# Performance work log

Measured on AMD Instinct MI355X. Metric: run time of the kernel, lower is better.

## Reference

```python
import jax, jax.numpy as jnp
import numpy as np
from jax import lax

A = 3          # anchors per scale
C = 80         # num foreground classes (COCO)
NMS_THRESH = 0.45
NMS_TOPK = 400
POST_NMS = 100


def setup_inputs() -> dict:
    key = jax.random.key(0)
    k0, k1, k2 = jax.random.split(key, 3)
    B = 8
    ch = A * (C + 5)  # 255
    # raw head outputs (pre-decode conv activations), modest scale so exp() stays sane
    tip0 = jax.random.normal(k0, (B, ch, 19, 19), jnp.float32) * 0.5
    tip1 = jax.random.normal(k1, (B, ch, 38, 38), jnp.float32) * 0.5
    tip2 = jax.random.normal(k2, (B, ch, 76, 76), jnp.float32) * 0.5
    # standard YOLOv3 COCO anchors, deepest scale (stride 32) first
    anchors0 = jnp.array([[116., 90.], [156., 198.], [373., 326.]], jnp.float32)
    anchors1 = jnp.array([[30., 61.], [62., 45.], [59., 119.]], jnp.float32)
    anchors2 = jnp.array([[10., 13.], [16., 30.], [33., 23.]], jnp.float32)
    return dict(tip0=tip0, tip1=tip1, tip2=tip2,
                anchors0=anchors0, anchors1=anchors1, anchors2=anchors2)


def _decode(tip, anchors, stride):
    """YOLOOutputV3 inference decode. tip: (B, A*(C+5), H, W)."""
    B, _, H, W = tip.shape
    # (B, A*(C+5), H*W) -> (B, H*W, A, C+5)
    pred = tip.reshape(B, A * (C + 5), H * W).transpose(0, 2, 1).reshape(B, H * W, A, C + 5)
    gx, gy = jnp.meshgrid(jnp.arange(W), jnp.arange(H))       # each (H, W)
    offsets = jnp.stack([gx, gy], -1).reshape(1, H * W, 1, 2).astype(tip.dtype)
    centers = (jax.nn.sigmoid(pred[..., :2]) + offsets) * stride          # (B,HW,A,2)
    scales = jnp.exp(pred[..., 2:4]) * anchors.reshape(1, 1, A, 2)        # (B,HW,A,2)
    conf = jax.nn.sigmoid(pred[..., 4:5])                                 # objectness
    cls_scores = jax.nn.sigmoid(pred[..., 5:]) * conf                      # (B,HW,A,C)
    wh = scales * 0.5
    bbox = jnp.concatenate([centers - wh, centers + wh], -1)               # corner format
    return bbox.reshape(B, H * W * A, 4), cls_scores.reshape(B, H * W * A, C)


def _pairwise_iou(b):
    """b: (K,4) corner boxes -> (K,K) IoU."""
    x1, y1, x2, y2 = b[:, 0], b[:, 1], b[:, 2], b[:, 3]
    area = jnp.maximum(x2 - x1, 0.) * jnp.maximum(y2 - y1, 0.)
    iw = jnp.maximum(jnp.minimum(x2[:, None], x2[None, :]) - jnp.maximum(x1[:, None], x1[None, :]), 0.)
    ih = jnp.maximum(jnp.minimum(y2[:, None], y2[None, :]) - jnp.maximum(y1[:, None], y1[None, :]), 0.)
    inter = iw * ih
    return inter / (area[:, None] + area[None, :] - inter + 1e-12)


def _nms_single(det):
    """Class-aware greedy NMS on one image. det: (M,6) = (cid, score, x1,y1,x2,y2)."""
    K = NMS_TOPK
    _, idx = lax.top_k(det[:, 1], K)     # sort by score, keep top K
    d = det[idx]                          # (K,6), descending score
    iou = _pairwise_iou(d[:, 2:6])
    same = d[:, 0][:, None] == d[:, 0][None, :]   # only same class suppresses
    valid = d[:, 1] > 0.
    rng = jnp.arange(K)

    def body(i, keep):
        sup = (iou[i] > NMS_THRESH) & same[i] & (rng > i) & keep[i] & valid[i]
        return keep & ~sup

    keep = lax.fori_loop(0, K, body, jnp.ones((K,), bool)) & valid
    d = jnp.where(keep[:, None], d, jnp.full_like(d, -1.))
    order = jnp.argsort(-d[:, 1])         # kept (sorted) first, suppressed (-1) last
    return d[order][:POST_NMS]            # (POST_NMS, 6)


def _detect(tip0, tip1, tip2, anchors0, anchors1, anchors2):
    dets = []
    for tip, anc, stride in ((tip0, anchors0, 32), (tip1, anchors1, 16), (tip2, anchors2, 8)):
        bbox, scores = _decode(tip, anc, stride)          # (B,N,4), (B,N,C)
        B, N, _ = bbox.shape
        ids = jnp.broadcast_to(jnp.arange(C, dtype=bbox.dtype)[None, None, :, None], (B, N, C, 1))
        sc = scores[..., None]                            # (B,N,C,1)
        bx = jnp.broadcast_to(bbox[:, :, None, :], (B, N, C, 4))
        dets.append(jnp.concatenate([ids, sc, bx], -1).reshape(B, N * C, 6))
    det = jnp.concatenate(dets, 1)                        # (B, M, 6)
    return jax.vmap(_nms_single)(det)                     # (B, POST_NMS, 6)


def reference(tip0, tip1, tip2, anchors0, anchors1, anchors2):
    res = _detect(tip0, tip1, tip2, anchors0, anchors1, anchors2)
    ids = res[..., 0:1]
    scores = res[..., 1:2]
    bboxes = res[..., 2:6]
    return ids, scores, bboxes
```

## Files before the change

kernel.cpp:

```cpp
#include <hip/hip_runtime.h>
#include <stdint.h>

#define NUMA 3
#define NUMC 80
#define CAP  49152
#define KTOP 400
#define POST 100
#define EQCAP 1024
#define PFCAP 2048
#define KEY0 0x3EE66666u
#define KEYTOP 0x3F800000u
#define LBUF 1024
#define NMASK (KTOP * 7)
#define CPB 20

typedef float f32x4 __attribute__((ext_vector_type(4)));

__device__ __forceinline__ float sigmoidf_(float x) { return 1.0f / (1.0f + expf(-x)); }
__device__ __forceinline__ unsigned uminu(unsigned a, unsigned b) { return a < b ? a : b; }

__device__ __forceinline__ float thr_for(float cf) {
    if (!(cf >= 0.45f)) return 3.0e38f;
    float q = 0.449f / cf;
    float r = q / (1.0f - q);
    return logf(r) - 0.01f;
}

__global__ __launch_bounds__(256) void score_main(
        const float* __restrict__ t0, const float* __restrict__ t1,
        const float* __restrict__ t2,
        unsigned* __restrict__ ccnt, unsigned* __restrict__ ckey,
        unsigned* __restrict__ cidx)
{
    __shared__ unsigned lkey[LBUF], lidx[LBUF];
    __shared__ unsigned lcnt, lbase;
    const int tid = threadIdx.x;
    if (tid == 0) lcnt = 0;
    __syncthreads();

    const int ba = blockIdx.z;
    const int b = ba / 3, a = ba - 3 * b;
    const int c0 = blockIdx.y * CPB;
    const int cx = blockIdx.x;

    #define LEMIT(SC, IDX) do { \
        unsigned key_ = __float_as_uint(SC); \
        if (key_ >= KEY0) { \
            unsigned pos_ = atomicAdd(&lcnt, 1u); \
            if (pos_ < LBUF) { lkey[pos_] = key_; lidx[pos_] = (IDX); } \
        } \
    } while (0)

    if (cx < 2) {
        const int hw = cx * 256 + tid;
        if (hw < 361) {
            const float* base = t0 + (size_t)(b * 255 + a * 85) * 361;
            float cr = base[4 * 361 + hw];
            const float* p0 = base + (size_t)(5 + c0) * 361 + hw;
            float xv[CPB];
            #pragma unroll
            for (int u = 0; u < CPB; u++) xv[u] = p0[u * 361];
            float cf = sigmoidf_(cr);
            float xt = thr_for(cf);
            unsigned ib = (unsigned)((hw * NUMA + a) * NUMC + c0);
            #pragma unroll
            for (int u = 0; u < CPB; u++)
                if (xv[u] > xt) LEMIT(sigmoidf_(xv[u]) * cf, ib + (unsigned)u);
        }
    } else {
        const float* tip; int vHW, v, candOff;
        if (cx < 4) { tip = t1; vHW = 361;  v = (cx - 2) * 256 + tid; candOff = 86640; }
        else        { tip = t2; vHW = 1444; v = (cx - 4) * 256 + tid; candOff = 433200; }
        if (v < vHW) {
            const f32x4* bp = (const f32x4*)(tip + (size_t)(b * 255 + a * 85) * (size_t)(vHW * 4));
            f32x4 cv = bp[(size_t)4 * vHW + v];
            const f32x4* p0 = bp + (size_t)(5 + c0) * vHW + v;
            f32x4 sv[CPB];
            #pragma unroll
            for (int u = 0; u < CPB; u++) sv[u] = p0[(size_t)u * vHW];
            float cf0 = sigmoidf_(cv[0]), cf1 = sigmoidf_(cv[1]);
            float cf2 = sigmoidf_(cv[2]), cf3 = sigmoidf_(cv[3]);
            float xt0 = thr_for(cf0), xt1 = thr_for(cf1);
            float xt2 = thr_for(cf2), xt3 = thr_for(cf3);
            unsigned ib0 = (unsigned)(candOff + (v * 4 * NUMA + a) * NUMC + c0);
            #pragma unroll
            for (int u = 0; u < CPB; u++) {
                unsigned ib = ib0 + (unsigned)u;
                if (sv[u][0] > xt0) LEMIT(sigmoidf_(sv[u][0]) * cf0, ib);
                if (sv[u][1] > xt1) LEMIT(sigmoidf_(sv[u][1]) * cf1, ib + 240);
                if (sv[u][2] > xt2) LEMIT(sigmoidf_(sv[u][2]) * cf2, ib + 480);
                if (sv[u][3] > xt3) LEMIT(sigmoidf_(sv[u][3]) * cf3, ib + 720);
            }
        }
    }
    #undef LEMIT

    __syncthreads();
    if (tid == 0) {
        unsigned c = lcnt;
        if (c > LBUF) {
            atomicOr(&ccnt[b], 0x80000000u);
            lbase = 0xFFFFFFFFu;
        } else {
            lbase = atomicAdd(&ccnt[b], c);
        }
    }
    __syncthreads();
    unsigned c = uminu(lcnt, (unsigned)LBUF);
    unsigned basep = lbase;
    if (basep != 0xFFFFFFFFu) {
        for (unsigned i = tid; i < c; i += 256) {
            unsigned p = basep + i;
            if (p < CAP) {
                ckey[(size_t)b * CAP + p] = lkey[i];
                cidx[(size_t)b * CAP + p] = lidx[i];
            }
        }
    }
}

__device__ __forceinline__ void wave_select(const unsigned* h, int nbins, unsigned rank,
                                            unsigned* resv, int tid)
{
    if (tid >= 64) return;
    const int lane = tid;
    const int cs = nbins >> 6;
    unsigned v = 0;
    for (int k = 0; k < cs; k++) {
        int off = (k + lane) & (cs - 1);
        v += h[lane * cs + off];
    }
    unsigned S = v;
    #pragma unroll
    for (int o = 1; o < 64; o <<= 1) {
        unsigned t = (unsigned)__shfl_down((int)S, o);
        if (lane + o < 64) S += t;
    }
    unsigned long long bm = __ballot(S >= rank);
    if (bm == 0ull) bm = 1ull;
    int C = 63 - __builtin_clzll(bm);
    unsigned SC = (unsigned)__builtin_amdgcn_readlane((int)S, C);
    unsigned vC = (unsigned)__builtin_amdgcn_readlane((int)v, C);
    unsigned rem = rank - (SC - vC);
    unsigned w = (lane < cs) ? h[C * cs + lane] : 0u;
    unsigned T = w;
    #pragma unroll
    for (int o = 1; o < 64; o <<= 1) {
        unsigned t = (unsigned)__shfl_down((int)T, o);
        if (lane + o < 64) T += t;
    }
    unsigned long long bm2 = __ballot((T >= rem) && (lane < cs));
    if (bm2 == 0ull) bm2 = 1ull;
    int B = 63 - __builtin_clzll(bm2);
    unsigned TB = (unsigned)__builtin_amdgcn_readlane((int)T, B);
    unsigned wB = (unsigned)__builtin_amdgcn_readlane((int)w, B);
    if (lane == 0) {
        resv[0] = (unsigned)(C * cs + B);
        resv[1] = rem - (TB - wB);
    }
}

__global__ __launch_bounds__(1024) void topk_sel(
        const float* __restrict__ t0, const float* __restrict__ t1,
        const float* __restrict__ t2,
        const float* __restrict__ anc0, const float* __restrict__ anc1,
        const float* __restrict__ anc2,
        const unsigned* __restrict__ ccnt,
        unsigned* __restrict__ ckey, unsigned* __restrict__ cidx,
        float* __restrict__ dX1, float* __restrict__ dY1,
        float* __restrict__ dX2, float* __restrict__ dY2,
        float* __restrict__ dSC, unsigned* __restrict__ dCID)
{
    const int b = blockIdx.x;
    const int tid = threadIdx.x;
    const int T = 1024;

    __shared__ unsigned hist[4096];
    __shared__ unsigned resv[2];
    __shared__ unsigned selk[512], seli[512];
    __shared__ unsigned eqi[EQCAP];
    __shared__ unsigned pk[PFCAP], pi[PFCAP];
    __shared__ unsigned cnts[3];
    __shared__ unsigned fcnt;

    unsigned* ck = ckey + (size_t)b * CAP;
    unsigned* ci = cidx + (size_t)b * CAP;
    unsigned nraw = ccnt[b];
    unsigned kbase = KEY0;

    if (!(nraw >= KTOP && nraw <= CAP)) {
        const int NPOS = 3 * (361 + 1444 + 5776);
        for (int i = tid; i < 2048; i += T) hist[i] = 0;
        if (tid == 0) fcnt = 0;
        __syncthreads();
        for (int p = tid; p < NPOS; p += T) {
            const float* tip; int HW, pp;
            if (p < 1083)      { tip = t0; HW = 361;  pp = p; }
            else if (p < 5415) { tip = t1; HW = 1444; pp = p - 1083; }
            else               { tip = t2; HW = 5776; pp = p - 5415; }
            int a = pp / HW, hwl = pp - a * HW;
            const float* base = tip + (size_t)(b * 255 + a * 85) * HW;
            float cf = sigmoidf_(base[4 * HW + hwl]);
            for (int u = 0; u < NUMC; u++) {
                float sc = sigmoidf_(base[(size_t)(5 + u) * HW + hwl]) * cf;
                atomicAdd(&hist[__float_as_uint(sc) >> 19], 1u);
            }
        }
        __syncthreads();
        wave_select(hist, 2048, KTOP, resv, tid);
        __syncthreads();
        unsigned cutkey = resv[0] << 19;
        __syncthreads();
        for (int p = tid; p < NPOS; p += T) {
            const float* tip; int HW, pp, candOff;
            if (p < 1083)      { tip = t0; HW = 361;  pp = p;        candOff = 0; }
            else if (p < 5415) { tip = t1; HW = 1444; pp = p - 1083; candOff = 86640; }
            else               { tip = t2; HW = 5776; pp = p - 5415; candOff = 433200; }
            int a = pp / HW, hwl = pp - a * HW;
            const float* base = tip + (size_t)(b * 255 + a * 85) * HW;
            float cf = sigmoidf_(base[4 * HW + hwl]);
            unsigned ib0 = (unsigned)(candOff + (hwl * NUMA + a) * NUMC);
            for (int u = 0; u < NUMC; u++) {
                float sc = sigmoidf_(base[(size_t)(5 + u) * HW + hwl]) * cf;
                unsigned key = __float_as_uint(sc);
                if (key >= cutkey) {
                    unsigned pos = atomicAdd(&fcnt, 1u);
                    if (pos < CAP) { ck[pos] = key; ci[pos] = ib0 + (unsigned)u; }
                }
            }
        }
        __syncthreads();
        nraw = fcnt;
        kbase = cutkey;
    }
    unsigned n = uminu(nraw, (unsigned)CAP);

    unsigned span = (KEYTOP - kbase) + 1u;
    unsigned SH = 0;
    while ((span >> SH) > 2047u) SH++;

    for (int i = tid; i < 2048; i += T) hist[i] = 0;
    __syncthreads();
    {
        unsigned n4 = n >> 2;
        const uint4* ck4 = (const uint4*)ck;
        for (unsigned i = tid; i < n4; i += T) {
            uint4 k = ck4[i];
            atomicAdd(&hist[(k.x - kbase) >> SH], 1u);
            atomicAdd(&hist[(k.y - kbase) >> SH], 1u);
            atomicAdd(&hist[(k.z - kbase) >> SH], 1u);
            atomicAdd(&hist[(k.w - kbase) >> SH], 1u);
        }
        for (unsigned i = (n4 << 2) + tid; i < n; i += T)
            atomicAdd(&hist[(ck[i] - kbase) >> SH], 1u);
    }
    __syncthreads();
    wave_select(hist, 2048, KTOP, resv, tid);
    __syncthreads();
    unsigned Bf = resv[0];
    __syncthreads();

    if (tid == 0) { cnts[0] = 0; cnts[1] = 0; cnts[2] = 0; }
    __syncthreads();
    for (unsigned i = tid; i < n; i += T) {
        unsigned k = ck[i];
        if (((k - kbase) >> SH) >= Bf) {
            unsigned q = atomicAdd(&cnts[2], 1u);
            if (q < (unsigned)PFCAP) { pk[q] = k; pi[q] = ci[i]; }
        }
    }
    __syncthreads();
    unsigned pfCnt = cnts[2];
    bool useP = (pfCnt <= (unsigned)PFCAP);
    unsigned m = useP ? pfCnt : n;

    for (int i = tid; i < 4096; i += T) hist[i] = 0;
    __syncthreads();
    for (unsigned i = tid; i < m; i += T) {
        unsigned k = useP ? pk[i] : ck[i];
        atomicAdd(&hist[k >> 19], 1u);
    }
    __syncthreads();
    wave_select(hist, 4096, KTOP, resv, tid);
    __syncthreads();
    unsigned b1 = resv[0], r2 = resv[1];
    __syncthreads();

    for (int i = tid; i < 4096; i += T) hist[i] = 0;
    __syncthreads();
    for (unsigned i = tid; i < m; i += T) {
        unsigned k = useP ? pk[i] : ck[i];
        if ((k >> 19) == b1) atomicAdd(&hist[(k >> 7) & 0xFFFu], 1u);
    }
    __syncthreads();
    wave_select(hist, 4096, r2, resv, tid);
    __syncthreads();
    unsigned b2 = resv[0], r3 = resv[1];
    __syncthreads();

    for (int i = tid; i < 128; i += T) hist[i] = 0;
    __syncthreads();
    unsigned pref = (b1 << 12) | b2;
    for (unsigned i = tid; i < m; i += T) {
        unsigned k = useP ? pk[i] : ck[i];
        if ((k >> 7) == pref) atomicAdd(&hist[k & 127u], 1u);
    }
    __syncthreads();
    wave_select(hist, 128, r3, resv, tid);
    __syncthreads();
    unsigned b3 = resv[0], needEq = resv[1];
    unsigned K400 = (b1 << 19) | (b2 << 7) | b3;
    __syncthreads();

    for (int i = tid; i < 512; i += T) { selk[i] = 0u; seli[i] = 0xFFFFFFFFu; }
    for (int i = tid; i < EQCAP; i += T) eqi[i] = 0xFFFFFFFFu;
    __syncthreads();
    for (unsigned i = tid; i < m; i += T) {
        unsigned k = useP ? pk[i] : ck[i];
        if (k > K400) {
            unsigned idx = useP ? pi[i] : ci[i];
            unsigned p = atomicAdd(&cnts[0], 1u);
            if (p < 512u) { selk[p] = k; seli[p] = idx; }
        } else if (k == K400) {
            unsigned idx = useP ? pi[i] : ci[i];
            unsigned q = atomicAdd(&cnts[1], 1u);
            if (q < (unsigned)EQCAP) eqi[q] = idx;
        }
    }
    __syncthreads();
    unsigned selCnt = uminu(cnts[0], (unsigned)KTOP);
    unsigned eqN   = uminu(cnts[1], (unsigned)EQCAP);

    if (eqN > needEq) {
        int P2 = 1; while ((unsigned)P2 < eqN) P2 <<= 1;
        for (int k2 = 2; k2 <= P2; k2 <<= 1) {
            for (int j = k2 >> 1; j > 0; j >>= 1) {
                __syncthreads();
                for (int i = tid; i < P2; i += T) {
                    int ixj = i ^ j;
                    if (ixj > i && ixj < P2) {
                        unsigned va = eqi[i], vb = eqi[ixj];
                        bool up = ((i & k2) == 0);
                        if (up ? (va > vb) : (va < vb)) { eqi[i] = vb; eqi[ixj] = va; }
                    }
                }
            }
        }
        __syncthreads();
    }
    for (unsigned t2v = tid; t2v < needEq; t2v += T) {
        unsigned p = selCnt + t2v;
        if (p < KTOP) { selk[p] = K400; seli[p] = eqi[t2v]; }
    }
    __syncthreads();

    for (int k2 = 2; k2 <= 512; k2 <<= 1) {
        int j = k2 >> 1;
        for (; j >= 64; j >>= 1) {
            __syncthreads();
            if (tid < 512) {
                int i = tid, ixj = i ^ j;
                if (ixj > i) {
                    unsigned ka = selk[i], kb = selk[ixj], ia = seli[i], ib = seli[ixj];
                    bool before = (ka > kb) || (ka == kb && ia < ib);
                    bool up = ((i & k2) == 0);
                    if (up ? !before : before) {
                        selk[i] = kb; selk[ixj] = ka; seli[i] = ib; seli[ixj] = ia;
                    }
                }
            }
        }
        __syncthreads();
        if (tid < 512) {
            for (; j > 0; j >>= 1) {
                int i = tid, ixj = i ^ j;
                if (ixj > i) {
                    unsigned ka = selk[i], kb = selk[ixj], ia = seli[i], ib = seli[ixj];
                    bool before = (ka > kb) || (ka == kb && ia < ib);
                    bool up = ((i & k2) == 0);
                    if (up ? !before : before) {
                        selk[i] = kb; selk[ixj] = ka; seli[i] = ib; seli[ixj] = ia;
                    }
                }
            }
        }
    }
    __syncthreads();

    if (tid < KTOP) {
        unsigned idx = seli[tid];
        int o = b * KTOP + tid;
        if (idx == 0xFFFFFFFFu) {
            dX1[o] = -1.f; dY1[o] = -1.f; dX2[o] = -1.f; dY2[o] = -1.f;
            dSC[o] = __uint_as_float(selk[tid]); dCID[o] = 0u;
        } else {
            const float* tip; const float* anc; int HW, W, candOff; float strideF;
            if (idx < 86640u)       { tip = t0; anc = anc0; HW = 361;  W = 19; strideF = 32.f; candOff = 0; }
            else if (idx < 433200u) { tip = t1; anc = anc1; HW = 1444; W = 38; strideF = 16.f; candOff = 86640; }
            else                    { tip = t2; anc = anc2; HW = 5776; W = 76; strideF = 8.f;  candOff = 433200; }
            unsigned local = idx - (unsigned)candOff;
            int cls = (int)(local % NUMC);
            int nn  = (int)(local / NUMC);
            int a = nn % NUMA, hwl = nn / NUMA;
            const float* base = tip + (size_t)(b * 255 + a * 85) * HW + hwl;
            float tx = base[0];
            float ty = base[(size_t)HW];
            float tw = base[(size_t)2 * HW];
            float th = base[(size_t)3 * HW];
            float fx = (float)(hwl % W), fy = (float)(hwl / W);
            float cx = (sigmoidf_(tx) + fx) * strideF;
            float cy = (sigmoidf_(ty) + fy) * strideF;
            float hw_ = expf(tw) * anc[2 * a]     * 0.5f;
            float hh_ = expf(th) * anc[2 * a + 1] * 0.5f;
            dX1[o] = cx - hw_; dY1[o] = cy - hh_;
            dX2[o] = cx + hw_; dY2[o] = cy + hh_;
            dSC[o] = __uint_as_float(selk[tid]);
            dCID[o] = (unsigned)cls;
        }
    }
}

__global__ __launch_bounds__(256) void mask_kernel(
        const float* __restrict__ dX1, const float* __restrict__ dY1,
        const float* __restrict__ dX2, const float* __restrict__ dY2,
        const unsigned* __restrict__ dCID, unsigned long long* __restrict__ maskG)
{
    __shared__ float lx1[KTOP], ly1[KTOP], lx2[KTOP], ly2[KTOP];
    __shared__ int lcid[KTOP];
    const int b = blockIdx.y;
    const int tid = threadIdx.x;
    for (int i = tid; i < KTOP; i += 256) {
        int o = b * KTOP + i;
        lx1[i] = dX1[o]; ly1[i] = dY1[o];
        lx2[i] = dX2[o]; ly2[i] = dY2[o];
        lcid[i] = (int)dCID[o];
    }
    __syncthreads();
    int p = blockIdx.x * 256 + tid;
    if (p < NMASK) {
        int i = p / 7, w = p - i * 7;
        float x1i = lx1[i], y1i = ly1[i], x2i = lx2[i], y2i = ly2[i];
        float ai = fmaxf(x2i - x1i, 0.f) * fmaxf(y2i - y1i, 0.f);
        int cidI = lcid[i];
        unsigned long long m = 0ull;
        int j0 = w * 64;
        int rot = (9 * w) & 63;
        for (int t = 0; t < 64; t++) {
            int j = j0 + ((t + rot) & 63);
            if (j >= KTOP || j <= i) continue;
            if (lcid[j] != cidI) continue;
            float iw = fminf(x2i, lx2[j]) - fmaxf(x1i, lx1[j]);
            float ih = fminf(y2i, ly2[j]) - fmaxf(y1i, ly1[j]);
            iw = fmaxf(iw, 0.f); ih = fmaxf(ih, 0.f);
            float inter = iw * ih;
            float aj = fmaxf(lx2[j] - lx1[j], 0.f) * fmaxf(ly2[j] - ly1[j], 0.f);
            float iou = inter / (ai + aj - inter + 1e-12f);
            if (iou > 0.45f) m |= (1ull << (j - j0));
        }
        maskG[(size_t)b * NMASK + p] = m;
    }
}

__global__ __launch_bounds__(512) void greedy_kernel(
        const float* __restrict__ dX1, const float* __restrict__ dY1,
        const float* __restrict__ dX2, const float* __restrict__ dY2,
        const float* __restrict__ dSC, const unsigned* __restrict__ dCID,
        const unsigned long long* __restrict__ maskG, float* __restrict__ out)
{
    __shared__ unsigned long long maskL[NMASK];
    __shared__ unsigned long long vkeep[7];
    __shared__ float oid[POST], osc[POST], obb[POST * 4];
    const int b = blockIdx.x;
    const int tid = threadIdx.x;

    for (int i = tid; i < NMASK; i += 512) maskL[i] = maskG[(size_t)b * NMASK + i];
    if (tid < POST) { oid[tid] = -1.f; osc[tid] = -1.f; }
    if (tid < POST * 4) obb[tid] = -1.f;
    __syncthreads();

    if (tid < 64) {
        const int lane = tid;
        unsigned long long keep = 0ull;
        if (lane < 7) keep = (lane == 6) ? 0xFFFFull : ~0ull;
        unsigned long long mb[8];
        #pragma unroll
        for (int k = 0; k < 8; k++)
            mb[k] = (lane < 7) ? maskL[k * 7 + lane] : 0ull;
        for (int ib = 0; ib < KTOP; ib += 8) {
            #pragma unroll
            for (int k = 0; k < 8; k++) {
                int i = ib + k;
                unsigned long long m = mb[k];
                int nf = ib + 8 + k;
                mb[k] = (lane < 7 && nf < KTOP) ? maskL[nf * 7 + lane] : 0ull;
                int w = i >> 6;
                unsigned klo = (unsigned)__builtin_amdgcn_readlane((int)(unsigned)(keep & 0xFFFFFFFFull), w);
                unsigned khi = (unsigned)__builtin_amdgcn_readlane((int)(unsigned)(keep >> 32), w);
                unsigned long long kw = ((unsigned long long)khi << 32) | klo;
                if ((kw >> (i & 63)) & 1ull) keep &= ~m;
            }
        }
        if (lane < 7) vkeep[lane] = keep;
    }
    __syncthreads();

    if (tid < KTOP) {
        int w = tid >> 6, bp = tid & 63;
        unsigned long long kw = vkeep[w];
        if ((kw >> bp) & 1ull) {
            int r = 0;
            for (int q = 0; q < w; q++) r += __popcll(vkeep[q]);
            r += __popcll(kw & ((1ull << bp) - 1ull));
            if (r < POST) {
                int o = b * KTOP + tid;
                oid[r] = (float)(int)dCID[o];
                osc[r] = dSC[o];
                obb[r * 4 + 0] = dX1[o];
                obb[r * 4 + 1] = dY1[o];
                obb[r * 4 + 2] = dX2[o];
                obb[r * 4 + 3] = dY2[o];
            }
        }
    }
    __syncthreads();
    if (tid < POST) {
        out[b * POST + tid]       = oid[tid];
        out[800 + b * POST + tid] = osc[tid];
    }
    if (tid < POST * 4) out[1600 + b * POST * 4 + tid] = obb[tid];
}

extern "C" void kernel_launch(void* const* d_in, const int* in_sizes, int n_in,
                              void* d_out, int out_size, void* d_ws, size_t ws_size,
                              hipStream_t stream)
{
    const float* tip0 = (const float*)d_in[0];
    const float* tip1 = (const float*)d_in[1];
    const float* tip2 = (const float*)d_in[2];
    const float* anc0 = (const float*)d_in[3];
    const float* anc1 = (const float*)d_in[4];
    const float* anc2 = (const float*)d_in[5];
    float* out = (float*)d_out;

    unsigned* ccnt = (unsigned*)d_ws;
    unsigned* ckey = ccnt + 8;
    unsigned* cidx = ckey + (size_t)8 * CAP;
    float*    dX1  = (float*)(cidx + (size_t)8 * CAP);
    float*    dY1  = dX1 + 8 * KTOP;
    float*    dX2  = dY1 + 8 * KTOP;
    float*    dY2  = dX2 + 8 * KTOP;
    float*    dSC  = dY2 + 8 * KTOP;
    unsigned* dCID = (unsigned*)(dSC + 8 * KTOP);
    unsigned long long* maskG = (unsigned long long*)(dCID + 8 * KTOP);

    hipMemsetAsync(ccnt, 0, 8 * sizeof(unsigned), stream);

    dim3 g(10, 80 / CPB, 24);
    score_main<<<g, 256, 0, stream>>>(tip0, tip1, tip2, ccnt, ckey, cidx);
    topk_sel<<<8, 1024, 0, stream>>>(tip0, tip1, tip2, anc0, anc1, anc2,
                                     ccnt, ckey, cidx,
                                     dX1, dY1, dX2, dY2, dSC, dCID);
    mask_kernel<<<dim3((NMASK + 255) / 256, 8), 256, 0, stream>>>(
        dX1, dY1, dX2, dY2, dCID, maskG);
    greedy_kernel<<<8, 512, 0, stream>>>(dX1, dY1, dX2, dY2, dSC, dCID, maskG, out);
}
```

Baseline: 189.5 us.

## Build score histogram during scoring pass and replace bitonic sort with rank sort

The scoring kernel now accumulates a per-batch 2048-bin histogram of candidate keys in shared memory and merges it into global memory, so the top-k kernel can load it instead of rescanning all candidates with atomics on the common path. The bitonic sort of 512 selected keys, with its many barriers, is replaced by a rank-counting sort where each thread counts how many elements precede it and scatters directly. This adds per-block shared atomics and global histogram atomics in the scoring kernel and an O(n^2) shared-memory read loop, in exchange for fewer syncs and passes in the single-block-per-batch top-k kernel.

```diff
diff --git a/kernel.cpp b/kernel.cpp
--- a/kernel.cpp
+++ b/kernel.cpp
@@ -13,6 +13,7 @@
 #define LBUF 1024
 #define NMASK (KTOP * 7)
 #define CPB 20
+#define NBIN 2048
 
 typedef float f32x4 __attribute__((ext_vector_type(4)));
 
@@ -29,13 +30,15 @@
 __global__ __launch_bounds__(256) void score_main(
         const float* __restrict__ t0, const float* __restrict__ t1,
         const float* __restrict__ t2,
-        unsigned* __restrict__ ccnt, unsigned* __restrict__ ckey,
-        unsigned* __restrict__ cidx)
+        unsigned* __restrict__ histN, unsigned* __restrict__ ccnt,
+        unsigned* __restrict__ ckey, unsigned* __restrict__ cidx)
 {
     __shared__ unsigned lkey[LBUF], lidx[LBUF];
+    __shared__ unsigned lh[NBIN];
     __shared__ unsigned lcnt, lbase;
     const int tid = threadIdx.x;
     if (tid == 0) lcnt = 0;
+    for (int i = tid; i < NBIN; i += 256) lh[i] = 0;
     __syncthreads();
 
     const int ba = blockIdx.z;
@@ -46,6 +49,7 @@
     #define LEMIT(SC, IDX) do { \
         unsigned key_ = __float_as_uint(SC); \
         if (key_ >= KEY0) { \
+            atomicAdd(&lh[(key_ - KEY0) >> 13], 1u); \
             unsigned pos_ = atomicAdd(&lcnt, 1u); \
             if (pos_ < LBUF) { lkey[pos_] = key_; lidx[pos_] = (IDX); } \
         } \
@@ -117,6 +121,11 @@
             }
         }
     }
+    unsigned* gh = histN + b * NBIN;
+    for (int i = tid; i < NBIN; i += 256) {
+        unsigned v2 = lh[i];
+        if (v2) atomicAdd(&gh[i], v2);
+    }
 }
 
 __device__ __forceinline__ void wave_select(const unsigned* h, int nbins, unsigned rank,
@@ -165,7 +174,7 @@
         const float* __restrict__ t2,
         const float* __restrict__ anc0, const float* __restrict__ anc1,
         const float* __restrict__ anc2,
-        const unsigned* __restrict__ ccnt,
+        const unsigned* __restrict__ histN, const unsigned* __restrict__ ccnt,
         unsigned* __restrict__ ckey, unsigned* __restrict__ cidx,
         float* __restrict__ dX1, float* __restrict__ dY1,
         float* __restrict__ dX2, float* __restrict__ dY2,
@@ -178,6 +187,7 @@
     __shared__ unsigned hist[4096];
     __shared__ unsigned resv[2];
     __shared__ unsigned selk[512], seli[512];
+    __shared__ unsigned sk2[512], si2[512];
     __shared__ unsigned eqi[EQCAP];
     __shared__ unsigned pk[PFCAP], pi[PFCAP];
     __shared__ unsigned cnts[3];
@@ -187,8 +197,10 @@
     unsigned* ci = cidx + (size_t)b * CAP;
     unsigned nraw = ccnt[b];
     unsigned kbase = KEY0;
-
-    if (!(nraw >= KTOP && nraw <= CAP)) {
+    unsigned SH = 13;
+
+    bool cold = !(nraw >= KTOP && nraw <= CAP);
+    if (cold) {
         const int NPOS = 3 * (361 + 1444 + 5776);
         for (int i = tid; i < 2048; i += T) hist[i] = 0;
         if (tid == 0) fcnt = 0;
@@ -232,16 +244,15 @@
         __syncthreads();
         nraw = fcnt;
         kbase = cutkey;
+        unsigned span = (KEYTOP - kbase) + 1u;
+        SH = 0;
+        while ((span >> SH) > 2047u) SH++;
     }
     unsigned n = uminu(nraw, (unsigned)CAP);
 
-    unsigned span = (KEYTOP - kbase) + 1u;
-    unsigned SH = 0;
-    while ((span >> SH) > 2047u) SH++;
-
-    for (int i = tid; i < 2048; i += T) hist[i] = 0;
-    __syncthreads();
-    {
+    if (cold) {
+        for (int i = tid; i < 2048; i += T) hist[i] = 0;
+        __syncthreads();
         unsigned n4 = n >> 2;
         const uint4* ck4 = (const uint4*)ck;
         for (unsigned i = tid; i < n4; i += T) {
@@ -253,6 +264,8 @@
         }
         for (unsigned i = (n4 << 2) + tid; i < n; i += T)
             atomicAdd(&hist[(ck[i] - kbase) >> SH], 1u);
+    } else {
+        for (int i = tid; i < 2048; i += T) hist[i] = histN[b * NBIN + i];
     }
     __syncthreads();
     wave_select(hist, 2048, KTOP, resv, tid);
@@ -354,45 +367,25 @@
     }
     __syncthreads();
 
-    for (int k2 = 2; k2 <= 512; k2 <<= 1) {
-        int j = k2 >> 1;
-        for (; j >= 64; j >>= 1) {
-            __syncthreads();
-            if (tid < 512) {
-                int i = tid, ixj = i ^ j;
-                if (ixj > i) {
-                    unsigned ka = selk[i], kb = selk[ixj], ia = seli[i], ib = seli[ixj];
-                    bool before = (ka > kb) || (ka == kb && ia < ib);
-                    bool up = ((i & k2) == 0);
-                    if (up ? !before : before) {
-                        selk[i] = kb; selk[ixj] = ka; seli[i] = ib; seli[ixj] = ia;
-                    }
-                }
-            }
-        }
-        __syncthreads();
-        if (tid < 512) {
-            for (; j > 0; j >>= 1) {
-                int i = tid, ixj = i ^ j;
-                if (ixj > i) {
-                    unsigned ka = selk[i], kb = selk[ixj], ia = seli[i], ib = seli[ixj];
-                    bool before = (ka > kb) || (ka == kb && ia < ib);
-                    bool up = ((i & k2) == 0);
-                    if (up ? !before : before) {
-                        selk[i] = kb; selk[ixj] = ka; seli[i] = ib; seli[ixj] = ia;
-                    }
-                }
-            }
-        }
+    if (tid < 512) {
+        unsigned ki = selk[tid], ii = seli[tid];
+        int r = 0;
+        #pragma unroll 8
+        for (int j = 0; j < 512; j++) {
+            unsigned kj = selk[j], ij = seli[j];
+            bool before = (kj > ki) || (kj == ki && ij < ii);
+            r += before ? 1 : 0;
+        }
+        if (r < 512) { sk2[r] = ki; si2[r] = ii; }
     }
     __syncthreads();
 
     if (tid < KTOP) {
-        unsigned idx = seli[tid];
+        unsigned idx = si2[tid];
         int o = b * KTOP + tid;
         if (idx == 0xFFFFFFFFu) {
             dX1[o] = -1.f; dY1[o] = -1.f; dX2[o] = -1.f; dY2[o] = -1.f;
-            dSC[o] = __uint_as_float(selk[tid]); dCID[o] = 0u;
+            dSC[o] = __uint_as_float(sk2[tid]); dCID[o] = 0u;
         } else {
             const float* tip; const float* anc; int HW, W, candOff; float strideF;
             if (idx < 86640u)       { tip = t0; anc = anc0; HW = 361;  W = 19; strideF = 32.f; candOff = 0; }
@@ -414,7 +407,7 @@
             float hh_ = expf(th) * anc[2 * a + 1] * 0.5f;
             dX1[o] = cx - hw_; dY1[o] = cy - hh_;
             dX2[o] = cx + hw_; dY2[o] = cy + hh_;
-            dSC[o] = __uint_as_float(selk[tid]);
+            dSC[o] = __uint_as_float(sk2[tid]);
             dCID[o] = (unsigned)cls;
         }
     }
@@ -542,23 +535,24 @@
     const float* anc2 = (const float*)d_in[5];
     float* out = (float*)d_out;
 
-    unsigned* ccnt = (unsigned*)d_ws;
-    unsigned* ckey = ccnt + 8;
-    unsigned* cidx = ckey + (size_t)8 * CAP;
-    float*    dX1  = (float*)(cidx + (size_t)8 * CAP);
-    float*    dY1  = dX1 + 8 * KTOP;
-    float*    dX2  = dY1 + 8 * KTOP;
-    float*    dY2  = dX2 + 8 * KTOP;
-    float*    dSC  = dY2 + 8 * KTOP;
-    unsigned* dCID = (unsigned*)(dSC + 8 * KTOP);
+    unsigned* histN = (unsigned*)d_ws;
+    unsigned* ccnt  = histN + 8 * NBIN;
+    unsigned* ckey  = ccnt + 8;
+    unsigned* cidx  = ckey + (size_t)8 * CAP;
+    float*    dX1   = (float*)(cidx + (size_t)8 * CAP);
+    float*    dY1   = dX1 + 8 * KTOP;
+    float*    dX2   = dY1 + 8 * KTOP;
+    float*    dY2   = dX2 + 8 * KTOP;
+    float*    dSC   = dY2 + 8 * KTOP;
+    unsigned* dCID  = (unsigned*)(dSC + 8 * KTOP);
     unsigned long long* maskG = (unsigned long long*)(dCID + 8 * KTOP);
 
-    hipMemsetAsync(ccnt, 0, 8 * sizeof(unsigned), stream);
+    hipMemsetAsync(histN, 0, (8 * NBIN + 8) * sizeof(unsigned), stream);
 
     dim3 g(10, 80 / CPB, 24);
-    score_main<<<g, 256, 0, stream>>>(tip0, tip1, tip2, ccnt, ckey, cidx);
+    score_main<<<g, 256, 0, stream>>>(tip0, tip1, tip2, histN, ccnt, ckey, cidx);
     topk_sel<<<8, 1024, 0, stream>>>(tip0, tip1, tip2, anc0, anc1, anc2,
-                                     ccnt, ckey, cidx,
+                                     histN, ccnt, ckey, cidx,
                                      dX1, dY1, dX2, dY2, dSC, dCID);
     mask_kernel<<<dim3((NMASK + 255) / 256, 8), 256, 0, stream>>>(
         dX1, dY1, dX2, dY2, dCID, maskG);
```

Result: slower. 195.9 us (+3.4%).
